# Optimization experiments

Measured on AMD Instinct MI355X. Metric: run time of the kernel, lower is better.

The kernel has to match this reference:

```python
import jax, jax.numpy as jnp
import numpy as np

B, P, D, H, L = 1024, 22, 3, 64, 4
HS = P + 1  # 22-dim one-hot atom type + 1 time channel
N = B * P


def _edges():
    # fully-connected directed edges (no self loops) per graph, batched with node offsets
    idx = np.arange(P)
    r, c = np.meshgrid(idx, idx, indexing='ij')
    m = r != c
    r0, c0 = r[m], c[m]
    off = (P * np.arange(B))[:, None]
    row = (r0[None, :] + off).reshape(-1)
    col = (c0[None, :] + off).reshape(-1)
    return row.astype(np.int32), col.astype(np.int32)


def setup_inputs() -> dict:
    key = jax.random.key(0)
    ks = jax.random.split(key, 12)
    s = 0.02
    row, col = _edges()
    return dict(
        input_array=jax.random.normal(ks[0], (B, P * D), jnp.float32),
        time_array=jax.random.uniform(ks[1], (B,), jnp.float32),
        emb_w=jax.random.normal(ks[2], (HS, H), jnp.float32) * s,
        emb_b=jnp.zeros((H,), jnp.float32),
        edge_w1=jax.random.normal(ks[3], (L, 2 * H + 2, H), jnp.float32) * s,
        edge_b1=jnp.zeros((L, H), jnp.float32),
        edge_w2=jax.random.normal(ks[4], (L, H, H), jnp.float32) * s,
        edge_b2=jnp.zeros((L, H), jnp.float32),
        node_w1=jax.random.normal(ks[5], (L, 2 * H, H), jnp.float32) * s,
        node_b1=jnp.zeros((L, H), jnp.float32),
        node_w2=jax.random.normal(ks[6], (L, H, H), jnp.float32) * s,
        node_b2=jnp.zeros((L, H), jnp.float32),
        cm_w1=jax.random.normal(ks[7], (L, H, H), jnp.float32) * s,
        cm_b1=jnp.zeros((L, H), jnp.float32),
        cm_w2=jax.random.normal(ks[8], (L, H, 1), jnp.float32) * 0.001,  # xavier gain=0.001 final layer
        cc_w1=jax.random.normal(ks[9], (L, H, H), jnp.float32) * s,
        cc_b1=jnp.zeros((L, H), jnp.float32),
        cc_w2=jax.random.normal(ks[10], (L, H, 1), jnp.float32) * 0.001,
        row=jnp.asarray(row),
        col=jnp.asarray(col),
    )


def reference(input_array, time_array, emb_w, emb_b, edge_w1, edge_b1, edge_w2, edge_b2,
              node_w1, node_b1, node_w2, node_b2, cm_w1, cm_b1, cm_w2,
              cc_w1, cc_b1, cc_w2, row, col):
    silu = jax.nn.silu
    x0 = input_array.reshape(N, D)
    # h_initial: one-hot atom types repeated over batch, plus time channel
    h = jnp.tile(jnp.eye(P, dtype=input_array.dtype), (B, 1))  # [N, 22]
    t = jnp.repeat(time_array[:, None], P, axis=1).reshape(N, 1)
    h = jnp.concatenate([h, t], axis=1)  # [N, 23]
    # edge_attr = squared distance at initial coords (fixed across layers)
    edge_attr = jnp.sum((x0[row] - x0[col]) ** 2, axis=1, keepdims=True)  # [E,1]
    h = h @ emb_w + emb_b  # embedding
    x = x0
    seg = lambda d: jax.ops.segment_sum(d, row, num_segments=N)
    for l in range(L):
        diff = x[row] - x[col]                                   # [E,3]
        radial = jnp.sum(diff ** 2, axis=1, keepdims=True)       # [E,1]
        coord_diff = diff / (jnp.sqrt(radial + 1e-8) + 1)
        e_in = jnp.concatenate([h[row], h[col], radial, edge_attr], axis=1)
        ef = silu(silu(e_in @ edge_w1[l] + edge_b1[l]) @ edge_w2[l] + edge_b2[l])  # [E,H]
        cross = jnp.cross(x[row], x[col])                        # [E,3]
        cross = cross / (jnp.sqrt(jnp.sum(cross ** 2, axis=1, keepdims=True) + 1e-8) + 1)
        cm = silu(ef @ cm_w1[l] + cm_b1[l]) @ cm_w2[l]           # [E,1]
        cc = silu(ef @ cc_w1[l] + cc_b1[l]) @ cc_w2[l]           # [E,1]
        trans = coord_diff * cm + cc * cross                     # [E,3]
        x = x + seg(trans)                                       # agg='sum'
        agg = jnp.concatenate([h, seg(ef)], axis=1)              # [N,2H]
        h = h + (silu(agg @ node_w1[l] + node_b1[l]) @ node_w2[l] + node_b2[l])  # recurrent
    vel = (x - x0).reshape(B, P, D)
    vel = vel - jnp.mean(vel, axis=1, keepdims=True)  # remove_mean
    return vel.reshape(B, P * D)
```

## Files before the change

### kernel.cpp

```cpp
#include <hip/hip_runtime.h>
#include <math.h>

#define PP 22
#define HH 64
#define NL 4
#define NE 462

typedef __attribute__((ext_vector_type(8))) short bf16x8;
typedef __attribute__((ext_vector_type(4))) float f32x4;

#define MFMA(A, B, C) __builtin_amdgcn_mfma_f32_16x16x32_bf16(A, B, C, 0, 0, 0)
#define WAVE_SYNC() asm volatile("s_waitcnt lgkmcnt(0)" ::: "memory")

__device__ __forceinline__ float silu_f(float v) { return v / (1.0f + __expf(-v)); }

__device__ __forceinline__ unsigned short f2bf(float x) {
    unsigned int u = __float_as_uint(x);
    u += 0x7fffu + ((u >> 16) & 1u);
    return (unsigned short)(u >> 16);
}
__device__ __forceinline__ float bf2f(unsigned short h) {
    return __uint_as_float(((unsigned int)h) << 16);
}

__global__ __launch_bounds__(64) void prep_w(const float* __restrict__ w2,
                                             const float* __restrict__ cm1,
                                             const float* __restrict__ cc1,
                                             unsigned short* __restrict__ ws)
{
    int blk = blockIdx.x;
    int nt = blk & 3, kt = (blk >> 2) & 1, mat = (blk >> 3) % 3, l = blk / 24;
    const float* src = (mat == 0 ? w2 : (mat == 1 ? cm1 : cc1)) + l * HH * HH;
    int lane = threadIdx.x;
    int n  = nt * 16 + (lane & 15);
    int kb = kt * 32 + (lane >> 4) * 8;
    unsigned short* dh = ws + blk * 1024 + lane * 8;
    unsigned short* dl = dh + 512;
#pragma unroll
    for (int j = 0; j < 8; ++j) {
        float v = src[(kb + j) * HH + n];
        unsigned short hi = f2bf(v);
        unsigned short lo = f2bf(v - bf2f(hi));
        dh[j] = hi;
        dl[j] = lo;
    }
}

__global__ __launch_bounds__(512, 2) void egnn_kernel(
    const float* __restrict__ input, const float* __restrict__ timev,
    const float* __restrict__ emb_w, const float* __restrict__ emb_b,
    const float* __restrict__ edge_w1, const float* __restrict__ edge_b1,
    const float* __restrict__ edge_b2,
    const float* __restrict__ node_w1, const float* __restrict__ node_b1,
    const float* __restrict__ node_w2, const float* __restrict__ node_b2,
    const float* __restrict__ cm_b1, const float* __restrict__ cm_w2,
    const float* __restrict__ cc_b1, const float* __restrict__ cc_w2,
    const unsigned short* __restrict__ wfr,
    float* __restrict__ out)
{
    const int g    = blockIdx.x;
    const int tid  = threadIdx.x;
    const int w    = tid >> 6;
    const int lane = tid & 63;
    const int n0   = lane & 15;
    const int kg   = lane >> 4;

    __shared__ __align__(16) unsigned short wlds[24 * 1024];
    __shared__ float sApre[PP][68];
    __shared__ float sBpre[PP][68];
    __shared__ float sh[PP][HH];
    __shared__ float sSeg[PP][HH];
    __shared__ float sx[PP][3], sx0[PP][3], sTr[PP][3];
    __shared__ float srad[NE], sea[NE];
    __shared__ float scd[NE][3], scr[NE][3];
    __shared__ __align__(16) unsigned int sEF[8][1024];
    __shared__ float sW128[HH], sW129[HH];
    __shared__ float smean[3];

    if (tid < PP * 3) {
        float v = input[g * (PP * 3) + tid];
        sx0[tid / 3][tid % 3] = v;
        sx [tid / 3][tid % 3] = v;
    }
    {
        float tg = timev[g];
        for (int i = w; i < PP; i += 8)
            sh[i][lane] = emb_w[i * HH + lane] + tg * emb_w[PP * HH + lane] + emb_b[lane];
    }
    __syncthreads();
    if (tid < NE) {
        int a = tid / 21, r = tid % 21;
        int b = (r < a) ? r : r + 1;
        float dx = sx0[a][0] - sx0[b][0];
        float dy = sx0[a][1] - sx0[b][1];
        float dz = sx0[a][2] - sx0[b][2];
        sea[tid] = dx * dx + dy * dy + dz * dz;
    }

    for (int l = 0; l < NL; ++l) {
        __syncthreads();
        {
            const uint4* src = (const uint4*)(wfr + (size_t)l * 24576);
            uint4* dst = (uint4*)wlds;
            for (int idx = tid; idx < 3072; idx += 512) dst[idx] = src[idx];
        }
        if (tid < HH)            sW128[tid]      = edge_w1[(l * 130 + 128) * HH + tid];
        else if (tid < 2 * HH)   sW129[tid - HH] = edge_w1[(l * 130 + 129) * HH + tid - HH];
        if (tid < NE) {
            int a = tid / 21, r = tid % 21;
            int b = (r < a) ? r : r + 1;
            float ax = sx[a][0], ay = sx[a][1], az = sx[a][2];
            float bx = sx[b][0], by = sx[b][1], bz = sx[b][2];
            float dx = ax - bx, dy = ay - by, dz = az - bz;
            float rad = dx * dx + dy * dy + dz * dz;
            srad[tid] = rad;
            float inv = 1.0f / (sqrtf(rad + 1e-8f) + 1.0f);
            scd[tid][0] = dx * inv; scd[tid][1] = dy * inv; scd[tid][2] = dz * inv;
            float cx = ay * bz - az * by;
            float cy = az * bx - ax * bz;
            float cz = ax * by - ay * bx;
            float cn = 1.0f / (sqrtf(cx * cx + cy * cy + cz * cz + 1e-8f) + 1.0f);
            scr[tid][0] = cx * cn; scr[tid][1] = cy * cn; scr[tid][2] = cz * cn;
        }
        {
            const float* W1 = edge_w1 + l * 130 * HH;
            const float* B1 = edge_b1 + l * HH;
            for (int i = w; i < PP; i += 8) {
                float a1 = B1[lane];
                float b1v = 0.0f;
                const float4* hr = (const float4*)&sh[i][0];
#pragma unroll 4
                for (int k4 = 0; k4 < 16; ++k4) {
                    float4 hv = hr[k4];
                    int k = k4 * 4;
                    a1  += hv.x * W1[(k + 0) * HH + lane] + hv.y * W1[(k + 1) * HH + lane]
                         + hv.z * W1[(k + 2) * HH + lane] + hv.w * W1[(k + 3) * HH + lane];
                    b1v += hv.x * W1[(64 + k + 0) * HH + lane] + hv.y * W1[(64 + k + 1) * HH + lane]
                         + hv.z * W1[(64 + k + 2) * HH + lane] + hv.w * W1[(64 + k + 3) * HH + lane];
                }
                sApre[i][lane] = a1;
                sBpre[i][lane] = b1v;
            }
        }
        float b2r[4], cmbr[4], ccbr[4], cm2r[4], cc2r[4];
#pragma unroll
        for (int nt = 0; nt < 4; ++nt) {
            int idx = l * HH + nt * 16 + n0;
            b2r[nt]  = edge_b2[idx];
            cmbr[nt] = cm_b1[idx];
            ccbr[nt] = cc_b1[idx];
            cm2r[nt] = cm_w2[idx];
            cc2r[nt] = cc_w2[idx];
        }
        __syncthreads();

        for (int a = w; a < PP; a += 8) {
            float seg[4] = {0.f, 0.f, 0.f, 0.f};
            float trl = 0.0f;

#pragma unroll
            for (int t = 0; t < 2; ++t) {
                int e  = t * 16 + n0;
                int ok = (e < 21);
                int b  = ok ? ((e < a) ? e : e + 1) : a;
                int ge = a * 21 + (ok ? e : 0);
                float radv = ok ? srad[ge] : 0.f;
                float eav  = ok ? sea[ge]  : 0.f;

                bf16x8 ahi[2], alo[2];
#pragma unroll
                for (int kt = 0; kt < 2; ++kt) {
                    int kb = kt * 32 + kg * 8;
                    const float* ap  = &sApre[a][kb];
                    const float* bp  = &sBpre[b][kb];
                    const float* w8p = &sW128[kb];
                    const float* w9p = &sW129[kb];
#pragma unroll
                    for (int j = 0; j < 8; ++j) {
                        float z = ap[j] + bp[j] + radv * w8p[j] + eav * w9p[j];
                        z = silu_f(z);
                        unsigned short hi = f2bf(z);
                        unsigned short lo = f2bf(z - bf2f(hi));
                        ahi[kt][j] = (short)hi;
                        alo[kt][j] = (short)lo;
                    }
                }

                f32x4 acc[4];
#pragma unroll
                for (int nt = 0; nt < 4; ++nt) acc[nt] = (f32x4){0.f, 0.f, 0.f, 0.f};
#pragma unroll
                for (int nt = 0; nt < 4; ++nt) {
#pragma unroll
                    for (int kt = 0; kt < 2; ++kt) {
                        int fb = (kt * 4 + nt) * 1024;
                        bf16x8 bhi = *(const bf16x8*)&wlds[fb + lane * 8];
                        bf16x8 blo = *(const bf16x8*)&wlds[fb + 512 + lane * 8];
                        acc[nt] = MFMA(ahi[kt], bhi, acc[nt]);
                        acc[nt] = MFMA(alo[kt], bhi, acc[nt]);
                        acc[nt] = MFMA(ahi[kt], blo, acc[nt]);
                    }
                }

#pragma unroll
                for (int nt = 0; nt < 4; ++nt) {
#pragma unroll
                    for (int r = 0; r < 4; ++r) {
                        int row = kg * 4 + r;
                        float v = silu_f(acc[nt][r] + b2r[nt]);
                        if (t * 16 + row >= 21) v = 0.f;
                        seg[nt] += v;
                        unsigned short hi = f2bf(v);
                        unsigned short lo = f2bf(v - bf2f(hi));
                        int col = (nt * 16 + n0) ^ ((row & 7) << 3);
                        sEF[w][row * 64 + col] = (unsigned int)hi | ((unsigned int)lo << 16);
                    }
                }
                WAVE_SYNC();

                bf16x8 ehi[2], elo[2];
#pragma unroll
                for (int kt = 0; kt < 2; ++kt) {
                    int cb = (kt * 32 + kg * 8) ^ ((n0 & 7) << 3);
                    const unsigned int* p = &sEF[w][n0 * 64 + cb];
                    uint4 u0 = *(const uint4*)p;
                    uint4 u1 = *(const uint4*)(p + 4);
                    unsigned int uu[8] = {u0.x, u0.y, u0.z, u0.w, u1.x, u1.y, u1.z, u1.w};
#pragma unroll
                    for (int j = 0; j < 8; ++j) {
                        ehi[kt][j] = (short)(uu[j] & 0xffffu);
                        elo[kt][j] = (short)(uu[j] >> 16);
                    }
                }
                WAVE_SYNC();

                f32x4 am[4], ac[4];
#pragma unroll
                for (int nt = 0; nt < 4; ++nt) {
                    am[nt] = (f32x4){0.f, 0.f, 0.f, 0.f};
                    ac[nt] = (f32x4){0.f, 0.f, 0.f, 0.f};
                }
#pragma unroll
                for (int nt = 0; nt < 4; ++nt) {
#pragma unroll
                    for (int kt = 0; kt < 2; ++kt) {
                        int fbm = ((2 + kt) * 4 + nt) * 1024;
                        int fbc = ((4 + kt) * 4 + nt) * 1024;
                        bf16x8 mhi = *(const bf16x8*)&wlds[fbm + lane * 8];
                        bf16x8 mlo = *(const bf16x8*)&wlds[fbm + 512 + lane * 8];
                        bf16x8 chi = *(const bf16x8*)&wlds[fbc + lane * 8];
                        bf16x8 clo = *(const bf16x8*)&wlds[fbc + 512 + lane * 8];
                        am[nt] = MFMA(ehi[kt], mhi, am[nt]);
                        am[nt] = MFMA(elo[kt], mhi, am[nt]);
                        am[nt] = MFMA(ehi[kt], mlo, am[nt]);
                        ac[nt] = MFMA(ehi[kt], chi, ac[nt]);
                        ac[nt] = MFMA(elo[kt], chi, ac[nt]);
                        ac[nt] = MFMA(ehi[kt], clo, ac[nt]);
                    }
                }

#pragma unroll
                for (int r = 0; r < 4; ++r) {
                    float pm = 0.f, pc = 0.f;
#pragma unroll
                    for (int nt = 0; nt < 4; ++nt) {
                        pm += silu_f(am[nt][r] + cmbr[nt]) * cm2r[nt];
                        pc += silu_f(ac[nt][r] + ccbr[nt]) * cc2r[nt];
                    }
#pragma unroll
                    for (int off = 1; off <= 8; off <<= 1) {
                        pm += __shfl_xor(pm, off);
                        pc += __shfl_xor(pc, off);
                    }
                    int erow = t * 16 + kg * 4 + r;
                    if (erow < 21 && n0 < 3) {
                        int ge2 = a * 21 + erow;
                        trl += scd[ge2][n0] * pm + pc * scr[ge2][n0];
                    }
                }
            }

#pragma unroll
            for (int nt = 0; nt < 4; ++nt) {
                seg[nt] += __shfl_xor(seg[nt], 16);
                seg[nt] += __shfl_xor(seg[nt], 32);
            }
            trl += __shfl_xor(trl, 16);
            trl += __shfl_xor(trl, 32);
            if (lane < 16) {
#pragma unroll
                for (int nt = 0; nt < 4; ++nt) sSeg[a][nt * 16 + lane] = seg[nt];
            }
            if (lane < 3) sTr[a][lane] = trl;
        }
        __syncthreads();

        {
            const float* NW1 = node_w1 + l * 128 * HH;
            const float* NB1 = node_b1 + l * HH;
            const float* NW2 = node_w2 + l * HH * HH;
            const float* NB2 = node_b2 + l * HH;
            for (int i = w; i < PP; i += 8) {
                float m1 = NB1[lane];
                const float4* hr4 = (const float4*)&sh[i][0];
                const float4* sr4 = (const float4*)&sSeg[i][0];
#pragma unroll 4
                for (int k4 = 0; k4 < 16; ++k4) {
                    float4 hv = hr4[k4];
                    float4 sv = sr4[k4];
                    int k = k4 * 4;
                    m1 += hv.x * NW1[(k + 0) * HH + lane] + hv.y * NW1[(k + 1) * HH + lane]
                        + hv.z * NW1[(k + 2) * HH + lane] + hv.w * NW1[(k + 3) * HH + lane];
                    m1 += sv.x * NW1[(64 + k + 0) * HH + lane] + sv.y * NW1[(64 + k + 1) * HH + lane]
                        + sv.z * NW1[(64 + k + 2) * HH + lane] + sv.w * NW1[(64 + k + 3) * HH + lane];
                }
                float* mb = (float*)&sEF[w][0];
                mb[lane] = silu_f(m1);
                WAVE_SYNC();
                float hacc = NB2[lane];
#pragma unroll 4
                for (int k4 = 0; k4 < 16; ++k4) {
                    float4 mv = *(const float4*)(mb + k4 * 4);
                    int k = k4 * 4;
                    hacc += mv.x * NW2[(k + 0) * HH + lane] + mv.y * NW2[(k + 1) * HH + lane]
                          + mv.z * NW2[(k + 2) * HH + lane] + mv.w * NW2[(k + 3) * HH + lane];
                }
                WAVE_SYNC();
                sh[i][lane] += hacc;
                if (lane < 3) sx[i][lane] += sTr[i][lane];
            }
        }
    }

    __syncthreads();
    if (tid < 3) {
        float s = 0.0f;
        for (int p = 0; p < PP; ++p) s += sx[p][tid] - sx0[p][tid];
        smean[tid] = s / (float)PP;
    }
    __syncthreads();
    if (tid < PP * 3) {
        int p = tid / 3, d = tid % 3;
        out[g * (PP * 3) + tid] = (sx[p][d] - sx0[p][d]) - smean[d];
    }
}

extern "C" void kernel_launch(void* const* d_in, const int* in_sizes, int n_in,
                              void* d_out, int out_size, void* d_ws, size_t ws_size,
                              hipStream_t stream) {
    const float* input   = (const float*)d_in[0];
    const float* timev   = (const float*)d_in[1];
    const float* emb_w   = (const float*)d_in[2];
    const float* emb_b   = (const float*)d_in[3];
    const float* edge_w1 = (const float*)d_in[4];
    const float* edge_b1 = (const float*)d_in[5];
    const float* edge_w2 = (const float*)d_in[6];
    const float* edge_b2 = (const float*)d_in[7];
    const float* node_w1 = (const float*)d_in[8];
    const float* node_b1 = (const float*)d_in[9];
    const float* node_w2 = (const float*)d_in[10];
    const float* node_b2 = (const float*)d_in[11];
    const float* cm_w1   = (const float*)d_in[12];
    const float* cm_b1   = (const float*)d_in[13];
    const float* cm_w2   = (const float*)d_in[14];
    const float* cc_w1   = (const float*)d_in[15];
    const float* cc_b1   = (const float*)d_in[16];
    const float* cc_w2   = (const float*)d_in[17];

    unsigned short* wsu = (unsigned short*)d_ws;
    prep_w<<<dim3(96), dim3(64), 0, stream>>>(edge_w2, cm_w1, cc_w1, wsu);

    float* out = (float*)d_out;
    egnn_kernel<<<dim3(1024), dim3(512), 0, stream>>>(
        input, timev, emb_w, emb_b, edge_w1, edge_b1, edge_b2,
        node_w1, node_b1, node_w2, node_b2, cm_b1, cm_w2, cc_b1, cc_w2,
        wsu, out);
}
```

Before: 914.0 us.

## Move node and edge-pre GEMMs to split-bf16 MFMA and pack edges densely

The per-node edge-input projections and the node MLP move from scalar FMA loops to bf16 hi/lo split MFMA, using weight fragments precomputed by an expanded prep kernel. The edge loop now runs over 29 dense 16-edge tiles instead of padding each node's 21 edges to 32, and segment sums are accumulated with LDS atomics. Weight fragments are read straight from global/L2 instead of staged in LDS, which frees shared memory and raises launch bounds to 4 blocks per CU. The risks are LDS atomic contention, global fragment load latency inside the MFMA loops, and slightly different rounding in the node path.

Result: slower. 1.366 ms (+49.5%).

```diff
diff --git a/kernel.cpp b/kernel.cpp
--- a/kernel.cpp
+++ b/kernel.cpp
@@ -5,12 +5,14 @@
 #define HH 64
 #define NL 4
 #define NE 462
+#define NTILE 29
+#define SST 68
+#define EST 72
 
 typedef __attribute__((ext_vector_type(8))) short bf16x8;
 typedef __attribute__((ext_vector_type(4))) float f32x4;
 
 #define MFMA(A, B, C) __builtin_amdgcn_mfma_f32_16x16x32_bf16(A, B, C, 0, 0, 0)
-#define WAVE_SYNC() asm volatile("s_waitcnt lgkmcnt(0)" ::: "memory")
 
 __device__ __forceinline__ float silu_f(float v) { return v / (1.0f + __expf(-v)); }
 
@@ -23,36 +25,50 @@
     return __uint_as_float(((unsigned int)h) << 16);
 }
 
-__global__ __launch_bounds__(64) void prep_w(const float* __restrict__ w2,
-                                             const float* __restrict__ cm1,
-                                             const float* __restrict__ cc1,
-                                             unsigned short* __restrict__ ws)
+#define LD8(dst, PTR) { \
+    float4 _a = *(const float4*)(PTR); float4 _b = *(const float4*)((PTR) + 4); \
+    dst[0]=_a.x; dst[1]=_a.y; dst[2]=_a.z; dst[3]=_a.w; \
+    dst[4]=_b.x; dst[5]=_b.y; dst[6]=_b.z; dst[7]=_b.w; }
+
+__global__ __launch_bounds__(64) void prep_w(
+    const float* __restrict__ edge_w1, const float* __restrict__ edge_w2,
+    const float* __restrict__ cm_w1, const float* __restrict__ cc_w1,
+    const float* __restrict__ node_w1, const float* __restrict__ node_w2,
+    unsigned short* __restrict__ ws)
 {
     int blk = blockIdx.x;
-    int nt = blk & 3, kt = (blk >> 2) & 1, mat = (blk >> 3) % 3, l = blk / 24;
-    const float* src = (mat == 0 ? w2 : (mat == 1 ? cm1 : cc1)) + l * HH * HH;
+    int nt = blk & 3, kt = (blk >> 2) & 1, mat = (blk >> 3) & 7, l = blk >> 6;
+    const float* src;
+    switch (mat) {
+        case 0: src = edge_w1 + l * 130 * HH; break;
+        case 1: src = edge_w1 + l * 130 * HH + 64 * HH; break;
+        case 2: src = edge_w2 + l * HH * HH; break;
+        case 3: src = cm_w1   + l * HH * HH; break;
+        case 4: src = cc_w1   + l * HH * HH; break;
+        case 5: src = node_w1 + l * 128 * HH; break;
+        case 6: src = node_w1 + l * 128 * HH + 64 * HH; break;
+        default: src = node_w2 + l * HH * HH; break;
+    }
     int lane = threadIdx.x;
     int n  = nt * 16 + (lane & 15);
     int kb = kt * 32 + (lane >> 4) * 8;
     unsigned short* dh = ws + blk * 1024 + lane * 8;
-    unsigned short* dl = dh + 512;
 #pragma unroll
     for (int j = 0; j < 8; ++j) {
         float v = src[(kb + j) * HH + n];
         unsigned short hi = f2bf(v);
         unsigned short lo = f2bf(v - bf2f(hi));
-        dh[j] = hi;
-        dl[j] = lo;
+        dh[j]       = hi;
+        dh[512 + j] = lo;
     }
 }
 
-__global__ __launch_bounds__(512, 2) void egnn_kernel(
+__global__ __launch_bounds__(512, 4) void egnn_kernel(
     const float* __restrict__ input, const float* __restrict__ timev,
     const float* __restrict__ emb_w, const float* __restrict__ emb_b,
     const float* __restrict__ edge_w1, const float* __restrict__ edge_b1,
     const float* __restrict__ edge_b2,
-    const float* __restrict__ node_w1, const float* __restrict__ node_b1,
-    const float* __restrict__ node_w2, const float* __restrict__ node_b2,
+    const float* __restrict__ node_b1, const float* __restrict__ node_b2,
     const float* __restrict__ cm_b1, const float* __restrict__ cm_w2,
     const float* __restrict__ cc_b1, const float* __restrict__ cc_w2,
     const unsigned short* __restrict__ wfr,
@@ -64,18 +80,18 @@
     const int lane = tid & 63;
     const int n0   = lane & 15;
     const int kg   = lane >> 4;
-
-    __shared__ __align__(16) unsigned short wlds[24 * 1024];
-    __shared__ float sApre[PP][68];
-    __shared__ float sBpre[PP][68];
-    __shared__ float sh[PP][HH];
-    __shared__ float sSeg[PP][HH];
-    __shared__ float sx[PP][3], sx0[PP][3], sTr[PP][3];
+    const int mtile = w >> 2;
+    const int ntw   = w & 3;
+
+    __shared__ float sApre[PP][SST], sBpre[PP][SST];
+    __shared__ float sh[PP][SST], sSeg[PP][SST];
     __shared__ float srad[NE], sea[NE];
     __shared__ float scd[NE][3], scr[NE][3];
-    __shared__ __align__(16) unsigned int sEF[8][1024];
+    __shared__ float sx[PP][3], sx0[PP][3], sTr[PP][4];
     __shared__ float sW128[HH], sW129[HH];
     __shared__ float smean[3];
+    __shared__ __align__(16) unsigned int sEF[8][16 * EST];
+    unsigned int* sM = &sEF[0][0];
 
     if (tid < PP * 3) {
         float v = input[g * (PP * 3) + tid];
@@ -87,6 +103,8 @@
         for (int i = w; i < PP; i += 8)
             sh[i][lane] = emb_w[i * HH + lane] + tg * emb_w[PP * HH + lane] + emb_b[lane];
     }
+    for (int idx = tid; idx < PP * SST; idx += 512) (&sSeg[0][0])[idx] = 0.f;
+    if (tid < PP * 4) (&sTr[0][0])[tid] = 0.f;
     __syncthreads();
     if (tid < NE) {
         int a = tid / 21, r = tid % 21;
@@ -98,14 +116,8 @@
     }
 
     for (int l = 0; l < NL; ++l) {
-        __syncthreads();
-        {
-            const uint4* src = (const uint4*)(wfr + (size_t)l * 24576);
-            uint4* dst = (uint4*)wlds;
-            for (int idx = tid; idx < 3072; idx += 512) dst[idx] = src[idx];
-        }
-        if (tid < HH)            sW128[tid]      = edge_w1[(l * 130 + 128) * HH + tid];
-        else if (tid < 2 * HH)   sW129[tid - HH] = edge_w1[(l * 130 + 129) * HH + tid - HH];
+        const unsigned short* wfl = wfr + (size_t)l * 65536;
+
         if (tid < NE) {
             int a = tid / 21, r = tid % 21;
             int b = (r < a) ? r : r + 1;
@@ -122,24 +134,50 @@
             float cn = 1.0f / (sqrtf(cx * cx + cy * cy + cz * cz + 1e-8f) + 1.0f);
             scr[tid][0] = cx * cn; scr[tid][1] = cy * cn; scr[tid][2] = cz * cn;
         }
+        if (tid < HH)          sW128[tid]      = edge_w1[(l * 130 + 128) * HH + tid];
+        else if (tid < 2 * HH) sW129[tid - HH] = edge_w1[(l * 130 + 129) * HH + tid - HH];
+
         {
-            const float* W1 = edge_w1 + l * 130 * HH;
-            const float* B1 = edge_b1 + l * HH;
-            for (int i = w; i < PP; i += 8) {
-                float a1 = B1[lane];
-                float b1v = 0.0f;
-                const float4* hr = (const float4*)&sh[i][0];
-#pragma unroll 4
-                for (int k4 = 0; k4 < 16; ++k4) {
-                    float4 hv = hr[k4];
-                    int k = k4 * 4;
-                    a1  += hv.x * W1[(k + 0) * HH + lane] + hv.y * W1[(k + 1) * HH + lane]
-                         + hv.z * W1[(k + 2) * HH + lane] + hv.w * W1[(k + 3) * HH + lane];
-                    b1v += hv.x * W1[(64 + k + 0) * HH + lane] + hv.y * W1[(64 + k + 1) * HH + lane]
-                         + hv.z * W1[(64 + k + 2) * HH + lane] + hv.w * W1[(64 + k + 3) * HH + lane];
-                }
-                sApre[i][lane] = a1;
-                sBpre[i][lane] = b1v;
+            int node = mtile * 16 + n0;
+            int crow = node < PP ? node : 0;
+            bool vn = node < PP;
+            bf16x8 hhi[2], hlo[2];
+#pragma unroll
+            for (int kt = 0; kt < 2; ++kt) {
+                float vv[8];
+                LD8(vv, &sh[crow][kt * 32 + kg * 8]);
+#pragma unroll
+                for (int j = 0; j < 8; ++j) {
+                    float z = vn ? vv[j] : 0.f;
+                    unsigned short hi = f2bf(z);
+                    hhi[kt][j] = (short)hi;
+                    hlo[kt][j] = (short)f2bf(z - bf2f(hi));
+                }
+            }
+            f32x4 accA = (f32x4){0.f,0.f,0.f,0.f};
+            f32x4 accB = (f32x4){0.f,0.f,0.f,0.f};
+#pragma unroll
+            for (int kt = 0; kt < 2; ++kt) {
+                const unsigned short* p0 = wfl + (0 * 8 + kt * 4 + ntw) * 1024 + lane * 8;
+                bf16x8 bhi = *(const bf16x8*)p0, blo = *(const bf16x8*)(p0 + 512);
+                accA = MFMA(hhi[kt], bhi, accA);
+                accA = MFMA(hlo[kt], bhi, accA);
+                accA = MFMA(hhi[kt], blo, accA);
+                const unsigned short* p1 = wfl + (1 * 8 + kt * 4 + ntw) * 1024 + lane * 8;
+                bf16x8 chi = *(const bf16x8*)p1, clo = *(const bf16x8*)(p1 + 512);
+                accB = MFMA(hhi[kt], chi, accB);
+                accB = MFMA(hlo[kt], chi, accB);
+                accB = MFMA(hhi[kt], clo, accB);
+            }
+            int col = ntw * 16 + n0;
+            float b1v = edge_b1[l * HH + col];
+#pragma unroll
+            for (int q = 0; q < 4; ++q) {
+                int m = mtile * 16 + kg * 4 + q;
+                if (m < PP) {
+                    sApre[m][col] = accA[q] + b1v;
+                    sBpre[m][col] = accB[q];
+                }
             }
         }
         float b2r[4], cmbr[4], ccbr[4], cm2r[4], cc2r[4];
@@ -154,185 +192,212 @@
         }
         __syncthreads();
 
-        for (int a = w; a < PP; a += 8) {
-            float seg[4] = {0.f, 0.f, 0.f, 0.f};
-            float trl = 0.0f;
-
-#pragma unroll
-            for (int t = 0; t < 2; ++t) {
-                int e  = t * 16 + n0;
-                int ok = (e < 21);
-                int b  = ok ? ((e < a) ? e : e + 1) : a;
-                int ge = a * 21 + (ok ? e : 0);
-                float radv = ok ? srad[ge] : 0.f;
-                float eav  = ok ? sea[ge]  : 0.f;
-
-                bf16x8 ahi[2], alo[2];
+        unsigned int* sEFw = &sEF[w][0];
+        for (int j = w; j < NTILE; j += 8) {
+            int e0 = j * 16;
+            int e = e0 + n0;
+            int ec = e < NE ? e : 0;
+            int a = ec / 21, r = ec - a * 21;
+            int b = (r < a) ? r : r + 1;
+            float radv = srad[ec], eav = sea[ec];
+
+            bf16x8 ahi[2], alo[2];
+#pragma unroll
+            for (int kt = 0; kt < 2; ++kt) {
+                int base = kt * 32 + kg * 8;
+                float av[8], bv[8], w8[8], w9[8];
+                LD8(av, &sApre[a][base]);
+                LD8(bv, &sBpre[b][base]);
+                LD8(w8, &sW128[base]);
+                LD8(w9, &sW129[base]);
+#pragma unroll
+                for (int j8 = 0; j8 < 8; ++j8) {
+                    float z = av[j8] + bv[j8] + radv * w8[j8] + eav * w9[j8];
+                    z = silu_f(z);
+                    unsigned short hi = f2bf(z);
+                    ahi[kt][j8] = (short)hi;
+                    alo[kt][j8] = (short)f2bf(z - bf2f(hi));
+                }
+            }
+
+#pragma unroll
+            for (int nt = 0; nt < 4; ++nt) {
+                f32x4 acc = (f32x4){0.f,0.f,0.f,0.f};
 #pragma unroll
                 for (int kt = 0; kt < 2; ++kt) {
-                    int kb = kt * 32 + kg * 8;
-                    const float* ap  = &sApre[a][kb];
-                    const float* bp  = &sBpre[b][kb];
-                    const float* w8p = &sW128[kb];
-                    const float* w9p = &sW129[kb];
-#pragma unroll
-                    for (int j = 0; j < 8; ++j) {
-                        float z = ap[j] + bp[j] + radv * w8p[j] + eav * w9p[j];
-                        z = silu_f(z);
-                        unsigned short hi = f2bf(z);
-                        unsigned short lo = f2bf(z - bf2f(hi));
-                        ahi[kt][j] = (short)hi;
-                        alo[kt][j] = (short)lo;
+                    const unsigned short* p = wfl + (2 * 8 + kt * 4 + nt) * 1024 + lane * 8;
+                    bf16x8 bhi = *(const bf16x8*)p, blo = *(const bf16x8*)(p + 512);
+                    acc = MFMA(ahi[kt], bhi, acc);
+                    acc = MFMA(alo[kt], bhi, acc);
+                    acc = MFMA(ahi[kt], blo, acc);
+                }
+                int col = nt * 16 + n0;
+#pragma unroll
+                for (int q = 0; q < 4; ++q) {
+                    int erow = kg * 4 + q;
+                    int gE = e0 + erow;
+                    bool vr = gE < NE;
+                    float v = silu_f(acc[q] + b2r[nt]);
+                    v = vr ? v : 0.f;
+                    if (vr) {
+                        int an = gE / 21;
+                        atomicAdd(&sSeg[an][col], v);
                     }
-                }
-
-                f32x4 acc[4];
-#pragma unroll
-                for (int nt = 0; nt < 4; ++nt) acc[nt] = (f32x4){0.f, 0.f, 0.f, 0.f};
-#pragma unroll
-                for (int nt = 0; nt < 4; ++nt) {
-#pragma unroll
-                    for (int kt = 0; kt < 2; ++kt) {
-                        int fb = (kt * 4 + nt) * 1024;
-                        bf16x8 bhi = *(const bf16x8*)&wlds[fb + lane * 8];
-                        bf16x8 blo = *(const bf16x8*)&wlds[fb + 512 + lane * 8];
-                        acc[nt] = MFMA(ahi[kt], bhi, acc[nt]);
-                        acc[nt] = MFMA(alo[kt], bhi, acc[nt]);
-                        acc[nt] = MFMA(ahi[kt], blo, acc[nt]);
+                    unsigned short hi = f2bf(v);
+                    unsigned short lo = f2bf(v - bf2f(hi));
+                    sEFw[erow * EST + col] = (unsigned)hi | ((unsigned)lo << 16);
+                }
+            }
+
+            bf16x8 ehi[2], elo[2];
+#pragma unroll
+            for (int kt = 0; kt < 2; ++kt) {
+                const unsigned int* p = &sEFw[n0 * EST + kt * 32 + kg * 8];
+                uint4 u0 = *(const uint4*)p;
+                uint4 u1 = *(const uint4*)(p + 4);
+                unsigned uu[8] = {u0.x, u0.y, u0.z, u0.w, u1.x, u1.y, u1.z, u1.w};
+#pragma unroll
+                for (int j8 = 0; j8 < 8; ++j8) {
+                    ehi[kt][j8] = (short)(uu[j8] & 0xffffu);
+                    elo[kt][j8] = (short)(uu[j8] >> 16);
+                }
+            }
+
+            float pm[4] = {0.f,0.f,0.f,0.f}, pc[4] = {0.f,0.f,0.f,0.f};
+#pragma unroll
+            for (int nt = 0; nt < 4; ++nt) {
+                f32x4 am = (f32x4){0.f,0.f,0.f,0.f};
+                f32x4 ac = (f32x4){0.f,0.f,0.f,0.f};
+#pragma unroll
+                for (int kt = 0; kt < 2; ++kt) {
+                    const unsigned short* pmw = wfl + (3 * 8 + kt * 4 + nt) * 1024 + lane * 8;
+                    const unsigned short* pcw = wfl + (4 * 8 + kt * 4 + nt) * 1024 + lane * 8;
+                    bf16x8 mhi = *(const bf16x8*)pmw, mlo = *(const bf16x8*)(pmw + 512);
+                    bf16x8 chi = *(const bf16x8*)pcw, clo = *(const bf16x8*)(pcw + 512);
+                    am = MFMA(ehi[kt], mhi, am);
+                    am = MFMA(elo[kt], mhi, am);
+                    am = MFMA(ehi[kt], mlo, am);
+                    ac = MFMA(ehi[kt], chi, ac);
+                    ac = MFMA(elo[kt], chi, ac);
+                    ac = MFMA(ehi[kt], clo, ac);
+                }
+#pragma unroll
+                for (int q = 0; q < 4; ++q) {
+                    pm[q] += silu_f(am[q] + cmbr[nt]) * cm2r[nt];
+                    pc[q] += silu_f(ac[q] + ccbr[nt]) * cc2r[nt];
+                }
+            }
+#pragma unroll
+            for (int q = 0; q < 4; ++q) {
+#pragma unroll
+                for (int off = 1; off <= 8; off <<= 1) {
+                    pm[q] += __shfl_xor(pm[q], off);
+                    pc[q] += __shfl_xor(pc[q], off);
+                }
+            }
+            if (n0 < 3) {
+#pragma unroll
+                for (int q = 0; q < 4; ++q) {
+                    int gE = e0 + kg * 4 + q;
+                    if (gE < NE) {
+                        int a2 = gE / 21;
+                        atomicAdd(&sTr[a2][n0], scd[gE][n0] * pm[q] + pc[q] * scr[gE][n0]);
                     }
                 }
-
-#pragma unroll
-                for (int nt = 0; nt < 4; ++nt) {
-#pragma unroll
-                    for (int r = 0; r < 4; ++r) {
-                        int row = kg * 4 + r;
-                        float v = silu_f(acc[nt][r] + b2r[nt]);
-                        if (t * 16 + row >= 21) v = 0.f;
-                        seg[nt] += v;
-                        unsigned short hi = f2bf(v);
-                        unsigned short lo = f2bf(v - bf2f(hi));
-                        int col = (nt * 16 + n0) ^ ((row & 7) << 3);
-                        sEF[w][row * 64 + col] = (unsigned int)hi | ((unsigned int)lo << 16);
-                    }
-                }
-                WAVE_SYNC();
-
-                bf16x8 ehi[2], elo[2];
-#pragma unroll
-                for (int kt = 0; kt < 2; ++kt) {
-                    int cb = (kt * 32 + kg * 8) ^ ((n0 & 7) << 3);
-                    const unsigned int* p = &sEF[w][n0 * 64 + cb];
-                    uint4 u0 = *(const uint4*)p;
-                    uint4 u1 = *(const uint4*)(p + 4);
-                    unsigned int uu[8] = {u0.x, u0.y, u0.z, u0.w, u1.x, u1.y, u1.z, u1.w};
-#pragma unroll
-                    for (int j = 0; j < 8; ++j) {
-                        ehi[kt][j] = (short)(uu[j] & 0xffffu);
-                        elo[kt][j] = (short)(uu[j] >> 16);
-                    }
-                }
-                WAVE_SYNC();
-
-                f32x4 am[4], ac[4];
-#pragma unroll
-                for (int nt = 0; nt < 4; ++nt) {
-                    am[nt] = (f32x4){0.f, 0.f, 0.f, 0.f};
-                    ac[nt] = (f32x4){0.f, 0.f, 0.f, 0.f};
-                }
-#pragma unroll
-                for (int nt = 0; nt < 4; ++nt) {
-#pragma unroll
-                    for (int kt = 0; kt < 2; ++kt) {
-                        int fbm = ((2 + kt) * 4 + nt) * 1024;
-                        int fbc = ((4 + kt) * 4 + nt) * 1024;
-                        bf16x8 mhi = *(const bf16x8*)&wlds[fbm + lane * 8];
-                        bf16x8 mlo = *(const bf16x8*)&wlds[fbm + 512 + lane * 8];
-                        bf16x8 chi = *(const bf16x8*)&wlds[fbc + lane * 8];
-                        bf16x8 clo = *(const bf16x8*)&wlds[fbc + 512 + lane * 8];
-                        am[nt] = MFMA(ehi[kt], mhi, am[nt]);
-                        am[nt] = MFMA(elo[kt], mhi, am[nt]);
-                        am[nt] = MFMA(ehi[kt], mlo, am[nt]);
-                        ac[nt] = MFMA(ehi[kt], chi, ac[nt]);
-                        ac[nt] = MFMA(elo[kt], chi, ac[nt]);
-                        ac[nt] = MFMA(ehi[kt], clo, ac[nt]);
-                    }
-                }
-
-#pragma unroll
-                for (int r = 0; r < 4; ++r) {
-                    float pm = 0.f, pc = 0.f;
-#pragma unroll
-                    for (int nt = 0; nt < 4; ++nt) {
-                        pm += silu_f(am[nt][r] + cmbr[nt]) * cm2r[nt];
-                        pc += silu_f(ac[nt][r] + ccbr[nt]) * cc2r[nt];
-                    }
-#pragma unroll
-                    for (int off = 1; off <= 8; off <<= 1) {
-                        pm += __shfl_xor(pm, off);
-                        pc += __shfl_xor(pc, off);
-                    }
-                    int erow = t * 16 + kg * 4 + r;
-                    if (erow < 21 && n0 < 3) {
-                        int ge2 = a * 21 + erow;
-                        trl += scd[ge2][n0] * pm + pc * scr[ge2][n0];
-                    }
-                }
-            }
-
-#pragma unroll
-            for (int nt = 0; nt < 4; ++nt) {
-                seg[nt] += __shfl_xor(seg[nt], 16);
-                seg[nt] += __shfl_xor(seg[nt], 32);
-            }
-            trl += __shfl_xor(trl, 16);
-            trl += __shfl_xor(trl, 32);
-            if (lane < 16) {
-#pragma unroll
-                for (int nt = 0; nt < 4; ++nt) sSeg[a][nt * 16 + lane] = seg[nt];
-            }
-            if (lane < 3) sTr[a][lane] = trl;
+            }
         }
         __syncthreads();
 
         {
-            const float* NW1 = node_w1 + l * 128 * HH;
-            const float* NB1 = node_b1 + l * HH;
-            const float* NW2 = node_w2 + l * HH * HH;
-            const float* NB2 = node_b2 + l * HH;
-            for (int i = w; i < PP; i += 8) {
-                float m1 = NB1[lane];
-                const float4* hr4 = (const float4*)&sh[i][0];
-                const float4* sr4 = (const float4*)&sSeg[i][0];
-#pragma unroll 4
-                for (int k4 = 0; k4 < 16; ++k4) {
-                    float4 hv = hr4[k4];
-                    float4 sv = sr4[k4];
-                    int k = k4 * 4;
-                    m1 += hv.x * NW1[(k + 0) * HH + lane] + hv.y * NW1[(k + 1) * HH + lane]
-                        + hv.z * NW1[(k + 2) * HH + lane] + hv.w * NW1[(k + 3) * HH + lane];
-                    m1 += sv.x * NW1[(64 + k + 0) * HH + lane] + sv.y * NW1[(64 + k + 1) * HH + lane]
-                        + sv.z * NW1[(64 + k + 2) * HH + lane] + sv.w * NW1[(64 + k + 3) * HH + lane];
-                }
-                float* mb = (float*)&sEF[w][0];
-                mb[lane] = silu_f(m1);
-                WAVE_SYNC();
-                float hacc = NB2[lane];
-#pragma unroll 4
-                for (int k4 = 0; k4 < 16; ++k4) {
-                    float4 mv = *(const float4*)(mb + k4 * 4);
-                    int k = k4 * 4;
-                    hacc += mv.x * NW2[(k + 0) * HH + lane] + mv.y * NW2[(k + 1) * HH + lane]
-                          + mv.z * NW2[(k + 2) * HH + lane] + mv.w * NW2[(k + 3) * HH + lane];
-                }
-                WAVE_SYNC();
-                sh[i][lane] += hacc;
-                if (lane < 3) sx[i][lane] += sTr[i][lane];
-            }
-        }
-    }
-
-    __syncthreads();
+            int node = mtile * 16 + n0;
+            int crow = node < PP ? node : 0;
+            bool vn = node < PP;
+            bf16x8 nhi[4], nlo[4];
+#pragma unroll
+            for (int kt = 0; kt < 4; ++kt) {
+                float vv[8];
+                const float* src = (kt < 2) ? &sh[crow][kt * 32 + kg * 8]
+                                            : &sSeg[crow][(kt - 2) * 32 + kg * 8];
+                LD8(vv, src);
+#pragma unroll
+                for (int j8 = 0; j8 < 8; ++j8) {
+                    float z = vn ? vv[j8] : 0.f;
+                    unsigned short hi = f2bf(z);
+                    nhi[kt][j8] = (short)hi;
+                    nlo[kt][j8] = (short)f2bf(z - bf2f(hi));
+                }
+            }
+            f32x4 acc = (f32x4){0.f,0.f,0.f,0.f};
+#pragma unroll
+            for (int kt = 0; kt < 4; ++kt) {
+                int mat = (kt < 2) ? 5 : 6;
+                int ktt = kt & 1;
+                const unsigned short* p = wfl + (mat * 8 + ktt * 4 + ntw) * 1024 + lane * 8;
+                bf16x8 bhi = *(const bf16x8*)p, blo = *(const bf16x8*)(p + 512);
+                acc = MFMA(nhi[kt], bhi, acc);
+                acc = MFMA(nlo[kt], bhi, acc);
+                acc = MFMA(nhi[kt], blo, acc);
+            }
+            int col = ntw * 16 + n0;
+            float nb1 = node_b1[l * HH + col];
+#pragma unroll
+            for (int q = 0; q < 4; ++q) {
+                int m = mtile * 16 + kg * 4 + q;
+                if (m < PP) {
+                    float v = silu_f(acc[q] + nb1);
+                    unsigned short hi = f2bf(v);
+                    unsigned short lo = f2bf(v - bf2f(hi));
+                    sM[m * EST + col] = (unsigned)hi | ((unsigned)lo << 16);
+                }
+            }
+        }
+        __syncthreads();
+
+        {
+            int node = mtile * 16 + n0;
+            int crow = node < PP ? node : 0;
+            bool vn = node < PP;
+            bf16x8 mh[2], ml[2];
+#pragma unroll
+            for (int kt = 0; kt < 2; ++kt) {
+                const unsigned int* p = &sM[crow * EST + kt * 32 + kg * 8];
+                uint4 u0 = *(const uint4*)p;
+                uint4 u1 = *(const uint4*)(p + 4);
+                unsigned uu[8] = {u0.x, u0.y, u0.z, u0.w, u1.x, u1.y, u1.z, u1.w};
+#pragma unroll
+                for (int j8 = 0; j8 < 8; ++j8) {
+                    unsigned uv = vn ? uu[j8] : 0u;
+                    mh[kt][j8] = (short)(uv & 0xffffu);
+                    ml[kt][j8] = (short)(uv >> 16);
+                }
+            }
+            f32x4 acc = (f32x4){0.f,0.f,0.f,0.f};
+#pragma unroll
+            for (int kt = 0; kt < 2; ++kt) {
+                const unsigned short* p = wfl + (7 * 8 + kt * 4 + ntw) * 1024 + lane * 8;
+                bf16x8 bhi = *(const bf16x8*)p, blo = *(const bf16x8*)(p + 512);
+                acc = MFMA(mh[kt], bhi, acc);
+                acc = MFMA(ml[kt], bhi, acc);
+                acc = MFMA(mh[kt], blo, acc);
+            }
+            int col = ntw * 16 + n0;
+            float nb2 = node_b2[l * HH + col];
+#pragma unroll
+            for (int q = 0; q < 4; ++q) {
+                int m = mtile * 16 + kg * 4 + q;
+                if (m < PP) sh[m][col] += acc[q] + nb2;
+            }
+        }
+        if (tid < PP * 4) {
+            int p = tid >> 2, d = tid & 3;
+            float v = sTr[p][d];
+            if (d < 3) sx[p][d] += v;
+            sTr[p][d] = 0.f;
+        }
+        for (int idx = tid; idx < PP * SST; idx += 512) (&sSeg[0][0])[idx] = 0.f;
+        __syncthreads();
+    }
+
     if (tid < 3) {
         float s = 0.0f;
         for (int p = 0; p < PP; ++p) s += sx[p][tid] - sx0[p][tid];
@@ -368,11 +433,11 @@
     const float* cc_w2   = (const float*)d_in[17];
 
     unsigned short* wsu = (unsigned short*)d_ws;
-    prep_w<<<dim3(96), dim3(64), 0, stream>>>(edge_w2, cm_w1, cc_w1, wsu);
+    prep_w<<<dim3(256), dim3(64), 0, stream>>>(edge_w1, edge_w2, cm_w1, cc_w1,
+                                               node_w1, node_w2, wsu);
 
     float* out = (float*)d_out;
     egnn_kernel<<<dim3(1024), dim3(512), 0, stream>>>(
         input, timev, emb_w, emb_b, edge_w1, edge_b1, edge_b2,
-        node_w1, node_b1, node_w2, node_b2, cm_b1, cm_w2, cc_b1, cc_w2,
-        wsu, out);
+        node_b1, node_b2, cm_b1, cm_w2, cc_b1, cc_w2, wsu, out);
 }
```
